# Kernel tuning notes

Hardware: AMD Instinct MI355X
Metric: run time of the kernel (lower is better)

Reference implementation:

```python
import jax, jax.numpy as jnp
import numpy as np

HID = 4096; H = 128; P = 64; N = 128; G = 8; K = 4; CH = 128
INTER = H * P                      # 8192
CONV_DIM = INTER + 2 * G * N       # 10240
PROJ = INTER + CONV_DIM + H        # 18560
EPS = 1e-5


def segsum(x):
    # stable segment-sum: out[..., i, j] = sum_{j < k <= i} x[..., k]; -inf above diagonal
    T = x.shape[-1]
    xe = jnp.repeat(x[..., None], T, axis=-1)          # [..., i, j] = x[..., i]
    strict = jnp.tril(jnp.ones((T, T), bool), -1)
    s = jnp.cumsum(jnp.where(strict, xe, 0.0), axis=-2)
    keep = jnp.tril(jnp.ones((T, T), bool), 0)
    return jnp.where(keep, s, -jnp.inf)


def setup_inputs() -> dict:
    key = jax.random.key(0)
    ks = jax.random.split(key, 6)
    b, L = 2, 2048
    hidden_states = jax.random.normal(ks[0], (b, L, HID), jnp.float32)
    in_proj_w = jax.random.normal(ks[1], (PROJ, HID), jnp.float32) * (HID ** -0.5)
    conv_w = jax.random.normal(ks[2], (CONV_DIM, 1, K), jnp.float32) * 0.2
    conv_b = jax.random.normal(ks[3], (CONV_DIM,), jnp.float32) * 0.02
    dt_bias = jnp.ones((H,), jnp.float32)
    A_log = jnp.log(jnp.arange(1, H + 1, dtype=jnp.float32))
    D = jnp.ones((H,), jnp.float32)
    norm_weight = jnp.ones((INTER,), jnp.float32)
    out_proj_w = jax.random.normal(ks[4], (HID, INTER), jnp.float32) * (INTER ** -0.5)
    return dict(hidden_states=hidden_states, in_proj_w=in_proj_w, conv_w=conv_w, conv_b=conv_b,
                dt_bias=dt_bias, A_log=A_log, D=D, norm_weight=norm_weight, out_proj_w=out_proj_w)


def _mamba2(hidden_states, in_proj_w, conv_w, conv_b, dt_bias, A_log, D, norm_weight, out_proj_w):
    b, L, _ = hidden_states.shape
    nchunk = L // CH  # seq_len chosen to be a multiple of chunk_size (pad_size = 0)

    # in_proj and split into gate | conv path (x,B,C) | dt
    proj = hidden_states @ in_proj_w.T
    gate, hBC, dt = jnp.split(proj, [INTER, INTER + CONV_DIM], axis=-1)

    # causal depthwise conv1d (padding k-1, truncate) + SiLU
    xp = jnp.pad(hBC.transpose(0, 2, 1), ((0, 0), (0, 0), (K - 1, 0)))
    xc = jax.lax.conv_general_dilated(xp, conv_w, (1,), 'VALID',
                                      feature_group_count=CONV_DIM,
                                      dimension_numbers=('NCW', 'OIW', 'NCW'))
    hBC = jax.nn.silu((xc + conv_b[None, :, None]).transpose(0, 2, 1))
    hs, Bx, Cx = jnp.split(hBC, [INTER, INTER + G * N], axis=-1)

    A = -jnp.exp(A_log)                      # [H]
    dt = jax.nn.softplus(dt + dt_bias)       # time_step_limit = (0, inf) -> clamp is no-op

    hs = hs.reshape(b, L, H, P)
    rep = H // G
    Bm = jnp.tile(Bx.reshape(b, L, G, N), (1, 1, rep, 1))   # matches torch .repeat
    Cm = jnp.tile(Cx.reshape(b, L, G, N), (1, 1, rep, 1))

    D_res = D[None, None, :, None] * hs      # [b,L,H,P]

    # discretize and chunk
    X = (hs * dt[..., None]).reshape(b, nchunk, CH, H, P)
    A_dt = (A[None, None, :] * dt).reshape(b, nchunk, CH, H).transpose(0, 3, 1, 2)  # [b,H,c,l]
    Bc = Bm.reshape(b, nchunk, CH, H, N)
    Cc = Cm.reshape(b, nchunk, CH, H, N)
    A_cs = jnp.cumsum(A_dt, axis=-1)

    # 1. intra-chunk (diagonal blocks)
    Lmat = jnp.exp(segsum(A_dt))                              # [b,H,c,l,s]
    Gm = jnp.einsum('bclhn,bcshn->bclsh', Cc, Bc)
    M = Gm * Lmat.transpose(0, 2, 3, 4, 1)                    # [b,c,l,s,H]
    Y_diag = jnp.einsum('bclsh,bcshp->bclhp', M, X)

    # 2. per-chunk states
    decay_states = jnp.exp(A_cs[..., -1:] - A_cs)             # [b,H,c,l]
    B_decay = Bc * decay_states.transpose(0, 2, 3, 1)[..., None]
    states = jnp.einsum('bclhn,bclhp->bchpn', B_decay, X)     # [b,c,H,P,N]

    # 3. inter-chunk recurrence
    states = jnp.concatenate([jnp.zeros_like(states[:, :1]), states], axis=1)
    A_last = jnp.pad(A_cs[..., -1], ((0, 0), (0, 0), (1, 0)))  # [b,H,c+1]
    decay_chunk = jnp.exp(segsum(A_last)).transpose(0, 3, 2, 1)  # [b,c+1,c+1,H]
    new_states = jnp.einsum('bzjh,bzhpn->bjhpn', decay_chunk, states)
    prev_states = new_states[:, :-1]                           # [b,c,H,P,N]

    # 4. state -> output
    sdo = jnp.exp(A_cs).transpose(0, 2, 3, 1)                  # [b,c,l,H]
    Y_off = jnp.einsum('bclhn,bchpn->bclhp', Cc, prev_states) * sdo[..., None]

    y = (Y_diag + Y_off).reshape(b, L, H, P) + D_res
    scan_out = y.reshape(b, L, INTER)

    # gated group RMSNorm (norm_before_gate=False: gate first, then group-RMS)
    xg = scan_out * jax.nn.silu(gate)
    xr = xg.reshape(b, L, G, INTER // G)
    xr = xr * jax.lax.rsqrt(jnp.mean(xr * xr, axis=-1, keepdims=True) + EPS)
    normed = xr.reshape(b, L, INTER) * norm_weight

    return normed @ out_proj_w.T


def reference(hidden_states, in_proj_w, conv_w, conv_b, dt_bias, A_log, D, norm_weight, out_proj_w):
    return _mamba2(hidden_states, in_proj_w, conv_w, conv_b, dt_bias, A_log, D, norm_weight, out_proj_w)
```

## Files before the change

### kernel.cpp

```cpp
#include <hip/hip_runtime.h>

#define NH 128
#define PD 64
#define NSD 128
#define NG 8
#define CHK 128
#define HIDD 4096
#define INTER_D 8192
#define CONV_D 10240
#define PROJ_D 18560
#define NPAD 18688
#define SEQ 2048
#define ROWS 4096
#define NCH 16

typedef __attribute__((ext_vector_type(8))) short bf16x8;
typedef __attribute__((ext_vector_type(4))) float f32x4;

__device__ __forceinline__ unsigned short f2bf(float f) {
  unsigned int u = __float_as_uint(f);
  u += 0x7FFF + ((u >> 16) & 1);
  return (unsigned short)(u >> 16);
}
__device__ __forceinline__ float bf2f(unsigned short s) {
  return __uint_as_float(((unsigned int)s) << 16);
}

__device__ __forceinline__ void gld16(const unsigned short* g, unsigned short* l) {
  __builtin_amdgcn_global_load_lds(
      (__attribute__((address_space(1))) const void*)g,
      (__attribute__((address_space(3))) void*)l, 16, 0, 0);
}

#define BAR() __builtin_amdgcn_s_barrier()
#define SCHED() __builtin_amdgcn_sched_barrier(0)
#define VMCNT(n) asm volatile("s_waitcnt vmcnt(" #n ")" ::: "memory")

__device__ __forceinline__ bf16x8 ldsfrag(const unsigned short* slot, int row, int kslot) {
  int byte = row * 128 + (((kslot ^ (row & 7)) << 4));
  return *(const bf16x8*)((const char*)slot + byte);
}

__global__ __launch_bounds__(256) void cvt_kernel(const float* __restrict__ in,
                                                  unsigned short* __restrict__ out,
                                                  size_t n) {
  size_t i = ((size_t)blockIdx.x * 256 + threadIdx.x) * 4;
  if (i < n) {
    float4 f = *(const float4*)(in + i);
    ushort4 o;
    o.x = f2bf(f.x); o.y = f2bf(f.y); o.z = f2bf(f.z); o.w = f2bf(f.w);
    *(ushort4*)(out + i) = o;
  }
}

template <int OUT_BF16>
__global__ __launch_bounds__(512, 2) void gemm256(const unsigned short* __restrict__ A,
                                                  const unsigned short* __restrict__ B,
                                                  unsigned short* __restrict__ outb,
                                                  float* __restrict__ outf,
                                                  int Nreal, int K) {
  __shared__ unsigned short lds[8][8192];
  int tid = threadIdx.x, l = tid & 63, w = tid >> 6;
  int wm = w >> 2, wn = w & 3;
  int il = l & 15, fog = l >> 4;
  int bid = blockIdx.x;
  int xcd = bid & 7, local = bid >> 3;
  int mt = xcd * 2 + (local & 1), nt = local >> 1;
  const unsigned short* Abase = A + (size_t)mt * 256 * K;
  const unsigned short* Bbase = B + (size_t)nt * 256 * K;
  int NT = K >> 6;

  f32x4 acc[2][2][4][2];
#pragma unroll
  for (int a = 0; a < 2; ++a)
#pragma unroll
    for (int b = 0; b < 2; ++b)
#pragma unroll
      for (int m = 0; m < 4; ++m)
#pragma unroll
        for (int n = 0; n < 2; ++n) acc[a][b][m][n] = (f32x4){0.f, 0.f, 0.f, 0.f};

  auto STG = [&](int tt, int ty) {
    if (tt < NT) {
      const unsigned short* g = ((ty & 1) ? Bbase : Abase) + (size_t)((ty >> 1) * 128) * K + tt * 64;
      unsigned short* sp = (unsigned short*)lds[(tt & 1) * 4 + ty];
#pragma unroll
      for (int j = 0; j < 2; ++j) {
        int row = (j * 8 + w) * 8 + (l >> 3);
        int scol = ((l & 7) ^ (row & 7)) * 8;
        gld16(g + (size_t)row * K + scol, sp + (j * 8 + w) * 512);
      }
    }
  };

#define LDA(SLOT)                                          \
  _Pragma("unroll") for (int mi = 0; mi < 4; ++mi)         \
  _Pragma("unroll") for (int kk = 0; kk < 2; ++kk)         \
      av[mi][kk] = ldsfrag(SLOT, wm * 64 + mi * 16 + il, kk * 4 + fog);
#define LDB(SLOT)                                          \
  _Pragma("unroll") for (int ni = 0; ni < 2; ++ni)         \
  _Pragma("unroll") for (int kk = 0; kk < 2; ++kk)         \
      bv[ni][kk] = ldsfrag(SLOT, wn * 32 + ni * 16 + il, kk * 4 + fog);
#define MFMA_PH(QM, QN)                                    \
  _Pragma("unroll") for (int mi = 0; mi < 4; ++mi)         \
  _Pragma("unroll") for (int ni = 0; ni < 2; ++ni)         \
  _Pragma("unroll") for (int kk = 0; kk < 2; ++kk)         \
      acc[QM][QN][mi][ni] = __builtin_amdgcn_mfma_f32_16x16x32_bf16( \
          av[mi][kk], bv[ni][kk], acc[QM][QN][mi][ni], 0, 0, 0);

  STG(0, 0); STG(0, 1); STG(0, 2); STG(0, 3); STG(1, 1); STG(1, 2);
  VMCNT(4);
  BAR(); SCHED();

  for (int t = 0; t < NT; ++t) {
    const unsigned short* sA0 = lds[(t & 1) * 4 + 0];
    const unsigned short* sB0 = lds[(t & 1) * 4 + 1];
    const unsigned short* sA1 = lds[(t & 1) * 4 + 2];
    const unsigned short* sB1 = lds[(t & 1) * 4 + 3];
    bf16x8 av[4][2], bv[2][2];
    LDA(sA0); LDB(sB0);
    STG(t + 1, 0);
    BAR(); SCHED();
    __builtin_amdgcn_s_setprio(1);
    MFMA_PH(0, 0);
    __builtin_amdgcn_s_setprio(0);
    SCHED(); BAR();
    LDA(sA1);
    STG(t + 1, 3);
    BAR(); SCHED();
    __builtin_amdgcn_s_setprio(1);
    MFMA_PH(1, 0);
    __builtin_amdgcn_s_setprio(0);
    SCHED(); BAR();
    LDB(sB1);
    STG(t + 2, 1);
    BAR(); SCHED();
    __builtin_amdgcn_s_setprio(1);
    MFMA_PH(1, 1);
    __builtin_amdgcn_s_setprio(0);
    SCHED(); BAR();
    LDA(sA0);
    STG(t + 2, 2);
    BAR(); SCHED();
    __builtin_amdgcn_s_setprio(1);
    MFMA_PH(0, 1);
    __builtin_amdgcn_s_setprio(0);
    SCHED();
    if (t < NT - 2) { VMCNT(4); } else { VMCNT(0); }
    BAR(); SCHED();
  }

  int rl = (l >> 4) * 4;
#pragma unroll
  for (int qm = 0; qm < 2; ++qm)
#pragma unroll
    for (int qn = 0; qn < 2; ++qn)
#pragma unroll
      for (int mi = 0; mi < 4; ++mi)
#pragma unroll
        for (int ni = 0; ni < 2; ++ni) {
          int grow = mt * 256 + qm * 128 + wm * 64 + mi * 16 + rl;
          int gcol = nt * 256 + qn * 128 + wn * 32 + ni * 16 + il;
          if (!OUT_BF16 || gcol < Nreal) {
#pragma unroll
            for (int r = 0; r < 4; ++r) {
              float v = acc[qm][qn][mi][ni][r];
              if (OUT_BF16)
                outb[(size_t)(grow + r) * Nreal + gcol] = f2bf(v);
              else
                outf[(size_t)(grow + r) * Nreal + gcol] = v;
            }
          }
        }
#undef LDA
#undef LDB
#undef MFMA_PH
}

__global__ __launch_bounds__(128) void dts_kernel(const unsigned short* __restrict__ proj,
                                                  const float* __restrict__ dt_bias,
                                                  const float* __restrict__ A_log,
                                                  float* __restrict__ dtg,
                                                  float* __restrict__ acsg) {
  int bc = blockIdx.x;
  int h = threadIdx.x;
  int b = bc >> 4, c = bc & 15;
  float A = -__expf(A_log[h]);
  float bias = dt_bias[h];
  float cum = 0.f;
  int row0 = b * SEQ + c * CHK;
  for (int ll = 0; ll < CHK; ++ll) {
    float x = bf2f(proj[(size_t)(row0 + ll) * PROJ_D + (PROJ_D - NH) + h]) + bias;
    float d = (x > 20.f) ? x : log1pf(expf(x));
    dtg[(size_t)(row0 + ll) * NH + h] = d;
    cum += A * d;
    acsg[(((size_t)bc * NH) + h) * CHK + ll] = cum;
  }
}

__global__ __launch_bounds__(256) void conv_kernel(const unsigned short* __restrict__ proj,
                                                   const float* __restrict__ cw,
                                                   const float* __restrict__ cb,
                                                   unsigned short* __restrict__ xbc) {
  int ch = blockIdx.x * 256 + threadIdx.x;
  int row = blockIdx.y;
  int b = row >> 11, ll = row & 2047;
  float acc = cb[ch];
#pragma unroll
  for (int k = 0; k < 4; ++k) {
    int l2 = ll - 3 + k;
    if (l2 >= 0)
      acc += bf2f(proj[(size_t)(b * SEQ + l2) * PROJ_D + INTER_D + ch]) * cw[ch * 4 + k];
  }
  float s = acc / (1.f + __expf(-acc));
  xbc[(size_t)row * CONV_D + ch] = f2bf(s);
}

__global__ __launch_bounds__(512) void e1a_kernel(const unsigned short* __restrict__ xbc,
                                                  const float* __restrict__ dtg,
                                                  const float* __restrict__ acsg,
                                                  float* __restrict__ yb) {
  int bid = blockIdx.x;
  int h = bid & 127, c = (bid >> 7) & 15, b = bid >> 11;
  int g = h & 7;
  int row0 = b * SEQ + c * CHK;
  __shared__ __align__(16) char smem[53248];
  unsigned short* Cst = (unsigned short*)smem;
  unsigned short* Bst = (unsigned short*)(smem + 10240);
  unsigned short* Mt = (unsigned short*)smem;
  unsigned short* XT = (unsigned short*)(smem + 34816);
  float* Acs = (float*)(smem + 52224);
  int tid = threadIdx.x, lane = tid & 63, wv = tid >> 6;
  int fo = (lane >> 4) * 8, il = lane & 15, rl = (lane >> 4) * 4;
  if (tid < 128) Acs[tid] = acsg[(((size_t)(b * NCH + c) * NH) + h) * CHK + tid];

  f32x4 gm[8];
#pragma unroll
  for (int i = 0; i < 8; ++i) gm[i] = (f32x4){0.f, 0.f, 0.f, 0.f};
  int srow = tid >> 2, scol = (tid & 3) * 8;
  for (int kc = 0; kc < 4; ++kc) {
    __syncthreads();
    *(int4*)(Cst + srow * 40 + scol) =
        *(const int4*)(xbc + (size_t)(row0 + srow) * CONV_D + INTER_D + NG * NSD + g * NSD + kc * 32 + scol);
    *(int4*)(Bst + srow * 40 + scol) =
        *(const int4*)(xbc + (size_t)(row0 + srow) * CONV_D + INTER_D + g * NSD + kc * 32 + scol);
    __syncthreads();
    bf16x8 a = *(const bf16x8*)&Cst[(wv * 16 + il) * 40 + fo];
#pragma unroll
    for (int ni = 0; ni < 8; ++ni) {
      bf16x8 bb = *(const bf16x8*)&Bst[(ni * 16 + il) * 40 + fo];
      gm[ni] = __builtin_amdgcn_mfma_f32_16x16x32_bf16(a, bb, gm[ni], 0, 0, 0);
    }
  }
  __syncthreads();
#pragma unroll
  for (int ni = 0; ni < 8; ++ni) {
    int s = ni * 16 + il;
#pragma unroll
    for (int r = 0; r < 4; ++r) {
      int ll = wv * 16 + rl + r;
      float v = (s <= ll) ? gm[ni][r] * __expf(Acs[ll] - Acs[s]) : 0.f;
      Mt[ll * 136 + s] = f2bf(v);
    }
  }
#pragma unroll
  for (int j = 0; j < 2; ++j) {
    int q = tid + j * 512;
    int ll = q >> 3, p0 = (q & 7) * 8;
    int row = row0 + ll;
    float dtv = dtg[(size_t)row * NH + h];
    int4 raw = *(const int4*)(xbc + (size_t)row * CONV_D + h * PD + p0);
    unsigned short* u = (unsigned short*)&raw;
#pragma unroll
    for (int e = 0; e < 8; ++e) XT[(p0 + e) * 136 + ll] = f2bf(bf2f(u[e]) * dtv);
  }
  __syncthreads();
  f32x4 yd[4];
#pragma unroll
  for (int i = 0; i < 4; ++i) yd[i] = (f32x4){0.f, 0.f, 0.f, 0.f};
#pragma unroll
  for (int ks = 0; ks < 4; ++ks) {
    bf16x8 a = *(const bf16x8*)&Mt[(wv * 16 + il) * 136 + ks * 32 + fo];
#pragma unroll
    for (int pi = 0; pi < 4; ++pi) {
      bf16x8 bb = *(const bf16x8*)&XT[(pi * 16 + il) * 136 + ks * 32 + fo];
      yd[pi] = __builtin_amdgcn_mfma_f32_16x16x32_bf16(a, bb, yd[pi], 0, 0, 0);
    }
  }
#pragma unroll
  for (int pi = 0; pi < 4; ++pi) {
    int p = pi * 16 + il;
#pragma unroll
    for (int r = 0; r < 4; ++r) {
      int ll = wv * 16 + rl + r;
      yb[(size_t)(row0 + ll) * INTER_D + h * PD + p] = yd[pi][r];
    }
  }
}

__global__ __launch_bounds__(256) void e1b_kernel(const unsigned short* __restrict__ xbc,
                                                  const float* __restrict__ dtg,
                                                  const float* __restrict__ acsg,
                                                  float* __restrict__ states) {
  int bid = blockIdx.x;
  int h = bid & 127, c = (bid >> 7) & 15, b = bid >> 11;
  int g = h & 7;
  int row0 = b * SEQ + c * CHK;
  __shared__ __align__(16) char smem[52736];
  unsigned short* XT = (unsigned short*)smem;
  unsigned short* BdT = (unsigned short*)(smem + 17408);
  float* Acs = (float*)(smem + 52224);
  int tid = threadIdx.x, lane = tid & 63, wv = tid >> 6;
  int fo = (lane >> 4) * 8, il = lane & 15, rl = (lane >> 4) * 4;
  if (tid < 128) Acs[tid] = acsg[(((size_t)(b * NCH + c) * NH) + h) * CHK + tid];
  __syncthreads();
#pragma unroll
  for (int j = 0; j < 4; ++j) {
    int q = tid + j * 256;
    int ll = q >> 3, p0 = (q & 7) * 8;
    int row = row0 + ll;
    float dtv = dtg[(size_t)row * NH + h];
    int4 raw = *(const int4*)(xbc + (size_t)row * CONV_D + h * PD + p0);
    unsigned short* u = (unsigned short*)&raw;
#pragma unroll
    for (int e = 0; e < 8; ++e) XT[(p0 + e) * 136 + ll] = f2bf(bf2f(u[e]) * dtv);
  }
#pragma unroll
  for (int j = 0; j < 8; ++j) {
    int q = tid + j * 256;
    int ll = q >> 4, n0 = (q & 15) * 8;
    float dec = __expf(Acs[CHK - 1] - Acs[ll]);
    int4 raw = *(const int4*)(xbc + (size_t)(row0 + ll) * CONV_D + INTER_D + g * NSD + n0);
    unsigned short* u = (unsigned short*)&raw;
#pragma unroll
    for (int e = 0; e < 8; ++e) BdT[(n0 + e) * 136 + ll] = f2bf(bf2f(u[e]) * dec);
  }
  __syncthreads();
  f32x4 st[8];
#pragma unroll
  for (int i = 0; i < 8; ++i) st[i] = (f32x4){0.f, 0.f, 0.f, 0.f};
#pragma unroll
  for (int ks = 0; ks < 4; ++ks) {
    bf16x8 a = *(const bf16x8*)&XT[(wv * 16 + il) * 136 + ks * 32 + fo];
#pragma unroll
    for (int ni = 0; ni < 8; ++ni) {
      bf16x8 bb = *(const bf16x8*)&BdT[(ni * 16 + il) * 136 + ks * 32 + fo];
      st[ni] = __builtin_amdgcn_mfma_f32_16x16x32_bf16(a, bb, st[ni], 0, 0, 0);
    }
  }
  size_t base = ((size_t)(b * NH + h) * NCH + c) * (PD * NSD);
#pragma unroll
  for (int ni = 0; ni < 8; ++ni) {
    int n = ni * 16 + il;
#pragma unroll
    for (int r = 0; r < 4; ++r) {
      int p = wv * 16 + rl + r;
      states[base + p * NSD + n] = st[ni][r];
    }
  }
}

__global__ __launch_bounds__(256) void e2_kernel(const float* __restrict__ acsg,
                                                 float* __restrict__ states) {
  int bh = blockIdx.x;
  int b = bh >> 7, h = bh & 127;
  int t = threadIdx.x;
  float S[32];
#pragma unroll
  for (int j = 0; j < 32; ++j) S[j] = 0.f;
  for (int c = 0; c < NCH; ++c) {
    float alast = acsg[(((size_t)(b * NCH + c) * NH) + h) * CHK + (CHK - 1)];
    float dec = __expf(alast);
    size_t base = ((size_t)bh * NCH + c) * (PD * NSD);
#pragma unroll
    for (int j = 0; j < 32; ++j) {
      size_t e = base + (size_t)j * 256 + t;
      float v = states[e];
      states[e] = S[j];
      S[j] = S[j] * dec + v;
    }
  }
}

__global__ __launch_bounds__(256) void e3_kernel(const unsigned short* __restrict__ xbc,
                                                 const float* __restrict__ acsg,
                                                 const float* __restrict__ states,
                                                 float* __restrict__ yb) {
  int bid = blockIdx.x;
  int h = bid & 127, c = (bid >> 7) & 15, b = bid >> 11;
  int g = h & 7;
  int row0 = b * SEQ + c * CHK;
  __shared__ __align__(16) char smem[52736];
  unsigned short* Ct = (unsigned short*)smem;
  unsigned short* Sp = (unsigned short*)(smem + 34816);
  float* Acs = (float*)(smem + 52224);
  int tid = threadIdx.x, lane = tid & 63, wv = tid >> 6;
  int fo = (lane >> 4) * 8, il = lane & 15, rl = (lane >> 4) * 4;
  if (tid < 128) Acs[tid] = acsg[(((size_t)(b * NCH + c) * NH) + h) * CHK + tid];
  size_t sbase = ((size_t)(b * NH + h) * NCH + c) * (PD * NSD);
#pragma unroll
  for (int j = 0; j < 8; ++j) {
    int q = tid + j * 256;
    int ll = q >> 4, n0 = (q & 15) * 8;
    *(int4*)(Ct + ll * 136 + n0) =
        *(const int4*)(xbc + (size_t)(row0 + ll) * CONV_D + INTER_D + NG * NSD + g * NSD + n0);
  }
#pragma unroll
  for (int j = 0; j < 4; ++j) {
    int q = tid + j * 256;
    int p = q >> 4, n0 = (q & 15) * 8;
    unsigned short tmp[8];
#pragma unroll
    for (int e = 0; e < 8; ++e) tmp[e] = f2bf(states[sbase + p * NSD + n0 + e]);
    *(int4*)(Sp + p * 136 + n0) = *(int4*)tmp;
  }
  __syncthreads();
  f32x4 yo[2][4];
#pragma unroll
  for (int i = 0; i < 2; ++i)
#pragma unroll
    for (int j = 0; j < 4; ++j) yo[i][j] = (f32x4){0.f, 0.f, 0.f, 0.f};
#pragma unroll
  for (int ks = 0; ks < 4; ++ks) {
    bf16x8 a0 = *(const bf16x8*)&Ct[(wv * 32 + il) * 136 + ks * 32 + fo];
    bf16x8 a1 = *(const bf16x8*)&Ct[(wv * 32 + 16 + il) * 136 + ks * 32 + fo];
#pragma unroll
    for (int pi = 0; pi < 4; ++pi) {
      bf16x8 bb = *(const bf16x8*)&Sp[(pi * 16 + il) * 136 + ks * 32 + fo];
      yo[0][pi] = __builtin_amdgcn_mfma_f32_16x16x32_bf16(a0, bb, yo[0][pi], 0, 0, 0);
      yo[1][pi] = __builtin_amdgcn_mfma_f32_16x16x32_bf16(a1, bb, yo[1][pi], 0, 0, 0);
    }
  }
#pragma unroll
  for (int mi = 0; mi < 2; ++mi)
#pragma unroll
    for (int pi = 0; pi < 4; ++pi)
#pragma unroll
      for (int r = 0; r < 4; ++r) {
        int ll = wv * 32 + mi * 16 + rl + r;
        int p = pi * 16 + il;
        size_t idx = (size_t)(row0 + ll) * INTER_D + h * PD + p;
        yb[idx] += yo[mi][pi][r] * __expf(Acs[ll]);
      }
}

__global__ __launch_bounds__(256) void fnorm_kernel(const float* __restrict__ yb,
                                                    const unsigned short* __restrict__ xbc,
                                                    const unsigned short* __restrict__ proj,
                                                    const float* __restrict__ Dp,
                                                    const float* __restrict__ nw,
                                                    unsigned short* __restrict__ normed) {
  int row = blockIdx.x >> 3;
  int gg = blockIdx.x & 7;
  int t = threadIdx.x;
  float v[4];
  float ss = 0.f;
#pragma unroll
  for (int j = 0; j < 4; ++j) {
    int ch = gg * 1024 + j * 256 + t;
    int h = ch >> 6;
    float yy = yb[(size_t)row * INTER_D + ch];
    float hs = bf2f(xbc[(size_t)row * CONV_D + ch]);
    float gt = bf2f(proj[(size_t)row * PROJ_D + ch]);
    float val = yy + Dp[h] * hs;
    val *= gt / (1.f + __expf(-gt));
    v[j] = val;
    ss += val * val;
  }
  __shared__ float sred[256];
  sred[t] = ss;
  __syncthreads();
  for (int ofs = 128; ofs > 0; ofs >>= 1) {
    if (t < ofs) sred[t] += sred[t + ofs];
    __syncthreads();
  }
  float rms = rsqrtf(sred[0] / 1024.f + 1e-5f);
#pragma unroll
  for (int j = 0; j < 4; ++j) {
    int ch = gg * 1024 + j * 256 + t;
    normed[(size_t)row * INTER_D + ch] = f2bf(v[j] * rms * nw[ch]);
  }
}

extern "C" void kernel_launch(void* const* d_in, const int* in_sizes, int n_in,
                              void* d_out, int out_size, void* d_ws, size_t ws_size,
                              hipStream_t stream) {
  (void)in_sizes; (void)n_in; (void)out_size; (void)ws_size;
  const float* hs = (const float*)d_in[0];
  const float* w1 = (const float*)d_in[1];
  const float* cw = (const float*)d_in[2];
  const float* cb = (const float*)d_in[3];
  const float* dtb = (const float*)d_in[4];
  const float* alog = (const float*)d_in[5];
  const float* Dp = (const float*)d_in[6];
  const float* nw = (const float*)d_in[7];
  const float* w2 = (const float*)d_in[8];
  float* out = (float*)d_out;
  char* ws = (char*)d_ws;

  unsigned short* hsb = (unsigned short*)(ws);
  unsigned short* w1b = (unsigned short*)(ws + 33554432);
  unsigned short* w2b = (unsigned short*)(ws + 186646528);
  unsigned short* proj = (unsigned short*)(ws + 253755392);
  unsigned short* xbc = (unsigned short*)(ws + 405798912);
  float* dtg = (float*)(ws + 489684992);
  float* acsg = (float*)(ws + 491782144);
  float* states = (float*)(ws + 493879296);
  float* yb = (float*)(ws + 628097024);
  unsigned short* normed = (unsigned short*)(ws);

  cvt_kernel<<<dim3(16384), dim3(256), 0, stream>>>(hs, hsb, (size_t)ROWS * HIDD);
  cvt_kernel<<<dim3(74240), dim3(256), 0, stream>>>(w1, w1b, (size_t)PROJ_D * HIDD);
  cvt_kernel<<<dim3(32768), dim3(256), 0, stream>>>(w2, w2b, (size_t)HIDD * INTER_D);

  gemm256<1><<<dim3(16 * 73), dim3(512), 0, stream>>>(hsb, w1b, proj, nullptr,
                                                      PROJ_D, HIDD);
  dts_kernel<<<dim3(32), dim3(128), 0, stream>>>(proj, dtb, alog, dtg, acsg);
  conv_kernel<<<dim3(40, 4096), dim3(256), 0, stream>>>(proj, cw, cb, xbc);
  e1a_kernel<<<dim3(4096), dim3(512), 0, stream>>>(xbc, dtg, acsg, yb);
  e1b_kernel<<<dim3(4096), dim3(256), 0, stream>>>(xbc, dtg, acsg, states);
  e2_kernel<<<dim3(256), dim3(256), 0, stream>>>(acsg, states);
  e3_kernel<<<dim3(4096), dim3(256), 0, stream>>>(xbc, acsg, states, yb);
  fnorm_kernel<<<dim3(32768), dim3(256), 0, stream>>>(yb, xbc, proj, Dp, nw, normed);
  gemm256<0><<<dim3(16 * 16), dim3(512), 0, stream>>>(normed, w2b, nullptr, out,
                                                      HIDD, INTER_D);
}
```

Before: 1.551 ms.

## Restructure GEMM ping-pong pipeline to hold both B fragments and drop A reload

```diff
diff --git a/kernel.cpp b/kernel.cpp
--- a/kernel.cpp
+++ b/kernel.cpp
@@ -81,15 +81,14 @@
         for (int n = 0; n < 2; ++n) acc[a][b][m][n] = (f32x4){0.f, 0.f, 0.f, 0.f};
 
   auto STG = [&](int tt, int ty) {
-    if (tt < NT) {
-      const unsigned short* g = ((ty & 1) ? Bbase : Abase) + (size_t)((ty >> 1) * 128) * K + tt * 64;
-      unsigned short* sp = (unsigned short*)lds[(tt & 1) * 4 + ty];
-#pragma unroll
-      for (int j = 0; j < 2; ++j) {
-        int row = (j * 8 + w) * 8 + (l >> 3);
-        int scol = ((l & 7) ^ (row & 7)) * 8;
-        gld16(g + (size_t)row * K + scol, sp + (j * 8 + w) * 512);
-      }
+    int tc = tt < NT ? tt : NT - 1;
+    const unsigned short* g = ((ty & 1) ? Bbase : Abase) + (size_t)((ty >> 1) * 128) * K + tc * 64;
+    unsigned short* sp = (unsigned short*)lds[(tt & 1) * 4 + ty];
+#pragma unroll
+    for (int j = 0; j < 2; ++j) {
+      int row = (j * 8 + w) * 8 + (l >> 3);
+      int scol = ((l & 7) ^ (row & 7)) * 8;
+      gld16(g + (size_t)row * K + scol, sp + (j * 8 + w) * 512);
     }
   };
 
@@ -97,19 +96,19 @@
   _Pragma("unroll") for (int mi = 0; mi < 4; ++mi)         \
   _Pragma("unroll") for (int kk = 0; kk < 2; ++kk)         \
       av[mi][kk] = ldsfrag(SLOT, wm * 64 + mi * 16 + il, kk * 4 + fog);
-#define LDB(SLOT)                                          \
+#define LDB(QN, SLOT)                                      \
   _Pragma("unroll") for (int ni = 0; ni < 2; ++ni)         \
   _Pragma("unroll") for (int kk = 0; kk < 2; ++kk)         \
-      bv[ni][kk] = ldsfrag(SLOT, wn * 32 + ni * 16 + il, kk * 4 + fog);
+      bv[QN][ni][kk] = ldsfrag(SLOT, wn * 32 + ni * 16 + il, kk * 4 + fog);
 #define MFMA_PH(QM, QN)                                    \
   _Pragma("unroll") for (int mi = 0; mi < 4; ++mi)         \
   _Pragma("unroll") for (int ni = 0; ni < 2; ++ni)         \
   _Pragma("unroll") for (int kk = 0; kk < 2; ++kk)         \
       acc[QM][QN][mi][ni] = __builtin_amdgcn_mfma_f32_16x16x32_bf16( \
-          av[mi][kk], bv[ni][kk], acc[QM][QN][mi][ni], 0, 0, 0);
-
-  STG(0, 0); STG(0, 1); STG(0, 2); STG(0, 3); STG(1, 1); STG(1, 2);
-  VMCNT(4);
+          av[mi][kk], bv[QN][ni][kk], acc[QM][QN][mi][ni], 0, 0, 0);
+
+  STG(0, 0); STG(0, 1); STG(0, 3); STG(0, 2);
+  VMCNT(2);
   BAR(); SCHED();
 
   for (int t = 0; t < NT; ++t) {
@@ -117,36 +116,31 @@
     const unsigned short* sB0 = lds[(t & 1) * 4 + 1];
     const unsigned short* sA1 = lds[(t & 1) * 4 + 2];
     const unsigned short* sB1 = lds[(t & 1) * 4 + 3];
-    bf16x8 av[4][2], bv[2][2];
-    LDA(sA0); LDB(sB0);
-    STG(t + 1, 0);
-    BAR(); SCHED();
+    bf16x8 av[4][2], bv[2][2][2];
+    LDA(sA0); LDB(0, sB0); LDB(1, sB1);
+    STG(t + 1, 0); STG(t + 1, 1);
+    BAR();
     __builtin_amdgcn_s_setprio(1);
     MFMA_PH(0, 0);
     __builtin_amdgcn_s_setprio(0);
-    SCHED(); BAR();
+    VMCNT(4);
+    BAR(); SCHED();
+    STG(t + 1, 3);
+    __builtin_amdgcn_s_setprio(1);
+    MFMA_PH(0, 1);
+    __builtin_amdgcn_s_setprio(0);
+    BAR();
     LDA(sA1);
-    STG(t + 1, 3);
-    BAR(); SCHED();
+    STG(t + 1, 2);
+    BAR();
     __builtin_amdgcn_s_setprio(1);
     MFMA_PH(1, 0);
     __builtin_amdgcn_s_setprio(0);
-    SCHED(); BAR();
-    LDB(sB1);
-    STG(t + 2, 1);
-    BAR(); SCHED();
+    BAR();
     __builtin_amdgcn_s_setprio(1);
     MFMA_PH(1, 1);
     __builtin_amdgcn_s_setprio(0);
-    SCHED(); BAR();
-    LDA(sA0);
-    STG(t + 2, 2);
-    BAR(); SCHED();
-    __builtin_amdgcn_s_setprio(1);
-    MFMA_PH(0, 1);
-    __builtin_amdgcn_s_setprio(0);
-    SCHED();
-    if (t < NT - 2) { VMCNT(4); } else { VMCNT(0); }
+    VMCNT(2);
     BAR(); SCHED();
   }
 
```

After: 1.511 ms. 1.03x faster.
